# Optimization experiments

Hardware: AMD Instinct MI355X
Metric: run time of the kernel (lower is better)

Reference implementation:

```python
import jax, jax.numpy as jnp
import numpy as np

# Model dims (match init_kwargs)
N = 150            # n_constituents
P = 16             # len(params)
HID = 50           # hidden
DE = 14            # De
DO = 10            # Do
NT = 5             # n_targets
B = 256            # batch
NR = N * (N - 1)   # 22350 directed edges


def _linear_params(key, fan_in, fan_out):
    # torch.nn.Linear default init: U(-1/sqrt(fan_in), 1/sqrt(fan_in))
    k1, k2 = jax.random.split(key)
    lim = 1.0 / np.sqrt(fan_in)
    W = jax.random.uniform(k1, (fan_out, fan_in), minval=-lim, maxval=lim, dtype=jnp.float32)
    b = jax.random.uniform(k2, (fan_out,), minval=-lim, maxval=lim, dtype=jnp.float32)
    return W, b


def setup_inputs() -> dict:
    key = jax.random.key(0)
    ks = jax.random.split(key, 10)
    # Edge list: itertools.product(range(N), range(N)) with r != s; Rr one-hot on r, Rs on s.
    pairs = np.array([(r, s) for r in range(N) for s in range(N) if r != s], dtype=np.int32)
    recv = jnp.asarray(pairs[:, 0])  # [NR]
    send = jnp.asarray(pairs[:, 1])  # [NR]

    x = jax.random.normal(ks[0], (B, P, N), dtype=jnp.float32)

    fr1_w, fr1_b = _linear_params(ks[1], 2 * P, HID)
    fr2_w, fr2_b = _linear_params(ks[2], HID, HID // 2)
    fr3_w, fr3_b = _linear_params(ks[3], HID // 2, DE)
    fo1_w, fo1_b = _linear_params(ks[4], P + DE, HID)
    fo2_w, fo2_b = _linear_params(ks[5], HID, HID // 2)
    fo3_w, fo3_b = _linear_params(ks[6], HID // 2, DO)
    fc1_w, fc1_b = _linear_params(ks[7], DO * N, HID)
    fc2_w, fc2_b = _linear_params(ks[8], HID, HID // 2)
    fc3_w, fc3_b = _linear_params(ks[9], HID // 2, NT)

    return dict(x=x, recv=recv, send=send,
                fr1_w=fr1_w, fr1_b=fr1_b, fr2_w=fr2_w, fr2_b=fr2_b, fr3_w=fr3_w, fr3_b=fr3_b,
                fo1_w=fo1_w, fo1_b=fo1_b, fo2_w=fo2_w, fo2_b=fo2_b, fo3_w=fo3_w, fo3_b=fo3_b,
                fc1_w=fc1_w, fc1_b=fc1_b, fc2_w=fc2_w, fc2_b=fc2_b, fc3_w=fc3_w, fc3_b=fc3_b)


def reference(x, recv, send,
              fr1_w, fr1_b, fr2_w, fr2_b, fr3_w, fr3_b,
              fo1_w, fo1_b, fo2_w, fo2_b, fo3_w, fo3_b,
              fc1_w, fc1_b, fc2_w, fc2_b, fc3_w, fc3_b):
    relu = jax.nn.relu
    b = x.shape[0]
    # tmul(x, Rr/Rs) with one-hot Rr/Rs == gather along the node axis
    Orr = x[:, :, recv]                                   # (B, P, NR)
    Ors = x[:, :, send]                                   # (B, P, NR)
    Bm = jnp.concatenate([Orr, Ors], axis=1)              # (B, 2P, NR)
    Bm = jnp.transpose(Bm, (0, 2, 1))                     # (B, NR, 2P)
    # relational MLP fr (ReLU branch)
    h = relu(jnp.einsum('bef,hf->beh', Bm, fr1_w) + fr1_b)
    h = relu(jnp.einsum('beh,gh->beg', h, fr2_w) + fr2_b)
    E = relu(jnp.einsum('beg,dg->bed', h, fr3_w) + fr3_b)  # (B, NR, De)
    # tmul(E, Rr^T) == scatter-add edge effects onto receiver nodes
    Ebar = jnp.zeros((b, N, E.shape[-1]), x.dtype).at[:, recv].add(E)  # (B, N, De)
    C = jnp.concatenate([jnp.transpose(x, (0, 2, 1)), Ebar], axis=-1)  # (B, N, P+De)
    # object MLP fo
    h = relu(jnp.einsum('bnf,hf->bnh', C, fo1_w) + fo1_b)
    h = relu(jnp.einsum('bnh,gh->bng', h, fo2_w) + fo2_b)
    O = relu(jnp.einsum('bng,dg->bnd', h, fo3_w) + fo3_b)  # (B, N, Do)
    # classifier fc (sum_O=False: flatten N*Do)
    flat = O.reshape(b, N * O.shape[-1])
    h = relu(flat @ fc1_w.T + fc1_b)
    h = relu(h @ fc2_w.T + fc2_b)
    out = h @ fc3_w.T + fc3_b                              # (B, n_targets)
    return out
```

## Files before the change

kernel.cpp:

```cpp
#include <hip/hip_runtime.h>

#define N_   150
#define P_   16
#define DE_  14
#define DO_  10
#define NT_  5
#define B_   256
#define NRE  22350
#define H2_  25
#define HID_ 50
#define RPW  5

typedef float    f32x4 __attribute__((ext_vector_type(4)));
typedef _Float16 f16x8 __attribute__((ext_vector_type(8)));
typedef _Float16 f16x4 __attribute__((ext_vector_type(4)));

typedef f16x8 f16x8_a __attribute__((may_alias));
typedef f16x4 f16x4_a __attribute__((may_alias));
typedef int2  int2_a  __attribute__((may_alias));
typedef f32x4 f32x4_a __attribute__((may_alias));

#define EBAR_OFF 0u
#define O_OFF    2457600u
#define XT_OFF   3225600u
#define W1E_OFF  4454400u
#define W1O_OFF  4458496u
#define W2E_OFF  4462592u
#define W2O_OFF  4466688u
#define W3E_OFF  4470784u
#define W3O_OFF  4471808u
#define B1E_OFF  4472832u
#define B1O_OFF  4473088u
#define B2E_OFF  4473344u
#define B2O_OFF  4473472u
#define B3E_OFF  4473600u
#define B3O_OFF  4473664u

__global__ __launch_bounds__(256) void prep_kernel(
    const float* __restrict__ x,
    const float* __restrict__ fr1_w, const float* __restrict__ fr1_b,
    const float* __restrict__ fr2_w, const float* __restrict__ fr2_b,
    const float* __restrict__ fr3_w, const float* __restrict__ fr3_b,
    const float* __restrict__ fo1_w, const float* __restrict__ fo1_b,
    const float* __restrict__ fo2_w, const float* __restrict__ fo2_b,
    const float* __restrict__ fo3_w, const float* __restrict__ fo3_b,
    char* __restrict__ ws)
{
    int tid = blockIdx.x * 256 + threadIdx.x;
    if (tid < 614400) {
        int b = tid / 2400; int rr = tid - b * 2400;
        int n = rr >> 4, p = rr & 15;
        ((_Float16*)(ws + XT_OFF))[tid] = (_Float16)x[b * 2400 + p * N_ + n];
        return;
    }
    int t = tid - 614400;
    if (t < 2048) { int n = t >> 5, k = t & 31;
        ((_Float16*)(ws + W1E_OFF))[t] = (_Float16)((n < 50) ? fr1_w[n * 32 + k] : 0.f); return; }
    t -= 2048;
    if (t < 2048) { int n = t >> 5, k = t & 31;
        ((_Float16*)(ws + W1O_OFF))[t] = (_Float16)((n < 50 && k < 30) ? fo1_w[n * 30 + k] : 0.f); return; }
    t -= 2048;
    if (t < 2048) { int n = t >> 6, k = t & 63;
        ((_Float16*)(ws + W2E_OFF))[t] = (_Float16)((n < 25 && k < 50) ? fr2_w[n * 50 + k] : 0.f); return; }
    t -= 2048;
    if (t < 2048) { int n = t >> 6, k = t & 63;
        ((_Float16*)(ws + W2O_OFF))[t] = (_Float16)((n < 25 && k < 50) ? fo2_w[n * 50 + k] : 0.f); return; }
    t -= 2048;
    if (t < 512) { int n = t >> 5, k = t & 31;
        ((_Float16*)(ws + W3E_OFF))[t] = (_Float16)((n < 14 && k < 25) ? fr3_w[n * 25 + k] : 0.f); return; }
    t -= 512;
    if (t < 512) { int n = t >> 5, k = t & 31;
        ((_Float16*)(ws + W3O_OFF))[t] = (_Float16)((n < 10 && k < 25) ? fo3_w[n * 25 + k] : 0.f); return; }
    t -= 512;
    if (t < 64) { ((float*)(ws + B1E_OFF))[t] = (t < 50) ? fr1_b[t] : 0.f; return; }
    t -= 64;
    if (t < 64) { ((float*)(ws + B1O_OFF))[t] = (t < 50) ? fo1_b[t] : 0.f; return; }
    t -= 64;
    if (t < 32) { ((float*)(ws + B2E_OFF))[t] = (t < 25) ? fr2_b[t] : 0.f; return; }
    t -= 32;
    if (t < 32) { ((float*)(ws + B2O_OFF))[t] = (t < 25) ? fo2_b[t] : 0.f; return; }
    t -= 32;
    if (t < 16) { ((float*)(ws + B3E_OFF))[t] = (t < 14) ? fr3_b[t] : 0.f; return; }
    t -= 16;
    if (t < 16) { ((float*)(ws + B3O_OFF))[t] = (t < 10) ? fo3_b[t] : 0.f; return; }
}

__device__ __forceinline__ unsigned pk2(float a, float b) {
    auto p = __builtin_amdgcn_cvt_pkrtz(a, b);
    return __builtin_bit_cast(unsigned, p);
}
__device__ __forceinline__ unsigned pkmax0(unsigned x, unsigned z) {
    unsigned r;
    asm("v_pk_max_f16 %0, %1, %2" : "=v"(r) : "v"(x), "v"(z));
    return r;
}

template<int CTRL>
__device__ __forceinline__ float dppadd(float v) {
    int s = __builtin_amdgcn_update_dpp(0, __builtin_bit_cast(int, v), CTRL, 0xF, 0xF, true);
    return v + __builtin_bit_cast(float, s);
}
__device__ __forceinline__ float dpp_sum16(float v) {
    v = dppadd<0x121>(v);
    v = dppadd<0x122>(v);
    v = dppadd<0x124>(v);
    v = dppadd<0x128>(v);
    return v;
}

__global__ __launch_bounds__(256) void edge_kernel(char* __restrict__ ws)
{
    const _Float16* __restrict__ xT = (const _Float16*)(ws + XT_OFF);
    const _Float16* __restrict__ W1 = (const _Float16*)(ws + W1E_OFF);
    const _Float16* __restrict__ W2 = (const _Float16*)(ws + W2E_OFF);
    const _Float16* __restrict__ W3 = (const _Float16*)(ws + W3E_OFF);
    const float* __restrict__ b1 = (const float*)(ws + B1E_OFF);
    const float* __restrict__ b2 = (const float*)(ws + B2E_OFF);
    const float* __restrict__ b3 = (const float*)(ws + B3E_OFF);
    float* __restrict__ Ebar = (float*)(ws + EBAR_OFF);

    const int t = threadIdx.x, lane = t & 63, wid = t >> 6;
    const int e16 = lane & 15, g = lane >> 4;

    __shared__ __align__(16) char s_lds[4][6144];
    char* L = s_lds[wid];

    const int gw = blockIdx.x * 4 + wid;
    const int b  = gw / 30;
    const int r0 = (gw - b * 30) * RPW;

    f16x4 A1r[4], A1s[4];
#pragma unroll
    for (int nt = 0; nt < 4; ++nt) {
        A1r[nt] = *(const f16x4*)&W1[(nt * 16 + e16) * 32 + g * 4];
        A1s[nt] = *(const f16x4*)&W1[(nt * 16 + e16) * 32 + 16 + g * 4];
    }
    f16x8 A2f[2][2], A3f;
#pragma unroll
    for (int nt = 0; nt < 2; ++nt)
#pragma unroll
        for (int kt = 0; kt < 2; ++kt)
            A2f[nt][kt] = *(const f16x8*)&W2[(nt * 16 + e16) * 64 + kt * 32 + g * 8];
    A3f = *(const f16x8*)&W3[e16 * 32 + g * 8];

    f32x4 Cb1[4], Cb2[2], Cb3;
#pragma unroll
    for (int nt = 0; nt < 4; ++nt) Cb1[nt] = *(const f32x4*)&b1[nt * 16 + g * 4];
#pragma unroll
    for (int nt = 0; nt < 2; ++nt) Cb2[nt] = *(const f32x4*)&b2[nt * 16 + g * 4];
    Cb3 = *(const f32x4*)&b3[g * 4];

    const char* xTb = (const char*)xT + b * 4800;
    const int laneoff = e16 * 32 + g * 8;
    const int wsub = (g >> 1) * 256 + e16 * 16 + 8 * (g & 1);
    const int rsub = g * 256 + e16 * 16;
    const unsigned zu = 0;

    for (int rr = 0; rr < RPW; ++rr) {
        const int r = r0 + rr;

        f16x4 Bxr = *(const f16x4_a*)(xTb + r * 32 + g * 8);
        f32x4 H1P[4];
#pragma unroll
        for (int nt = 0; nt < 4; ++nt)
            H1P[nt] = __builtin_amdgcn_mfma_f32_16x16x16f16(A1r[nt], Bxr, Cb1[nt], 0, 0, 0);

        const int ktile = r >> 4, klane = r & 15;
        float ac0 = 0.f, ac1 = 0.f, ac2 = 0.f, ac3 = 0.f;

#pragma unroll 2
        for (int tile = 0; tile < 10; ++tile) {
            char* h1b = L + (tile & 1) * 3072;
            char* h2b = h1b + 2048;

            f16x4 Bxs = *(const f16x4_a*)(xTb + tile * 512 + laneoff);

#pragma unroll
            for (int nt = 0; nt < 4; ++nt) {
                f32x4 d1 = __builtin_amdgcn_mfma_f32_16x16x16f16(A1s[nt], Bxs, H1P[nt], 0, 0, 0);
                int2 pw;
                pw.x = (int)pkmax0(pk2(d1[0], d1[1]), zu);
                pw.y = (int)pkmax0(pk2(d1[2], d1[3]), zu);
                *(int2_a*)(h1b + nt * 512 + wsub) = pw;
            }

            f16x8 B2a = *(const f16x8_a*)(h1b + rsub);
            f16x8 B2b = *(const f16x8_a*)(h1b + 1024 + rsub);
#pragma unroll
            for (int nt = 0; nt < 2; ++nt) {
                f32x4 d2 = __builtin_amdgcn_mfma_f32_16x16x32_f16(A2f[nt][0], B2a, Cb2[nt], 0, 0, 0);
                d2 = __builtin_amdgcn_mfma_f32_16x16x32_f16(A2f[nt][1], B2b, d2, 0, 0, 0);
                int2 pw;
                pw.x = (int)pkmax0(pk2(d2[0], d2[1]), zu);
                pw.y = (int)pkmax0(pk2(d2[2], d2[3]), zu);
                *(int2_a*)(h2b + nt * 512 + wsub) = pw;
            }

            f16x8 B3f = *(const f16x8_a*)(h2b + rsub);
            f32x4 d3 = __builtin_amdgcn_mfma_f32_16x16x32_f16(A3f, B3f, Cb3, 0, 0, 0);

            float v0 = fmaxf(d3[0], 0.f), v1 = fmaxf(d3[1], 0.f);
            float v2 = fmaxf(d3[2], 0.f), v3 = fmaxf(d3[3], 0.f);
            if (tile == ktile || tile == 9) {
                bool kill = (tile == ktile && e16 == klane) || (tile == 9 && e16 >= 6);
                if (kill) { v0 = 0.f; v1 = 0.f; v2 = 0.f; v3 = 0.f; }
            }
            ac0 += v0; ac1 += v1; ac2 += v2; ac3 += v3;
        }

        ac0 = dpp_sum16(ac0); ac1 = dpp_sum16(ac1);
        ac2 = dpp_sum16(ac2); ac3 = dpp_sum16(ac3);
        if (e16 == 0) {
            f32x4 o = { ac0, ac1, ac2, ac3 };
            *(f32x4_a*)&Ebar[(b * 150 + r) * 16 + g * 4] = o;
        }
    }
}

__global__ __launch_bounds__(256) void obj_kernel(char* __restrict__ ws)
{
    const _Float16* __restrict__ xT = (const _Float16*)(ws + XT_OFF);
    const _Float16* __restrict__ W1 = (const _Float16*)(ws + W1O_OFF);
    const _Float16* __restrict__ W2 = (const _Float16*)(ws + W2O_OFF);
    const _Float16* __restrict__ W3 = (const _Float16*)(ws + W3O_OFF);
    const float* __restrict__ b1 = (const float*)(ws + B1O_OFF);
    const float* __restrict__ b2 = (const float*)(ws + B2O_OFF);
    const float* __restrict__ b3 = (const float*)(ws + B3O_OFF);
    const float* __restrict__ Ebar = (const float*)(ws + EBAR_OFF);
    _Float16* __restrict__ O = (_Float16*)(ws + O_OFF);

    const int t = threadIdx.x, lane = t & 63, wid = t >> 6;
    const int e16 = lane & 15, g = lane >> 4;

    __shared__ __align__(16) char s_lds[4][3072];
    char* ldsw = s_lds[wid];
    const int wsub = (g >> 1) * 256 + e16 * 16 + (g & 1) * 8;
    char*       h1w = ldsw + wsub;
    char*       h2w = ldsw + 2048 + wsub;
    const int rsub = g * 256 + e16 * 16;
    const char* h1r = ldsw + rsub;
    const char* h2r = ldsw + 2048 + rsub;

    f16x8 A1[4], A2[2][2], A3;
#pragma unroll
    for (int nt = 0; nt < 4; ++nt)
        A1[nt] = *(const f16x8*)&W1[(nt * 16 + e16) * 32 + g * 8];
#pragma unroll
    for (int nt = 0; nt < 2; ++nt)
#pragma unroll
        for (int kt = 0; kt < 2; ++kt)
            A2[nt][kt] = *(const f16x8*)&W2[(nt * 16 + e16) * 64 + kt * 32 + g * 8];
    A3 = *(const f16x8*)&W3[e16 * 32 + g * 8];

    f32x4 C1[4], C2[2];
#pragma unroll
    for (int nt = 0; nt < 4; ++nt) C1[nt] = *(const f32x4*)&b1[nt * 16 + g * 4];
#pragma unroll
    for (int nt = 0; nt < 2; ++nt) C2[nt] = *(const f32x4*)&b2[nt * 16 + g * 4];
    const float b3v = b3[e16];
    const f32x4 C3 = { b3v, b3v, b3v, b3v };
    const unsigned zu = 0;

    const int tile = blockIdx.x * 4 + wid;
    const int m = tile * 16 + e16;

    f16x8 Bf;
    if (g < 2) {
        Bf = *(const f16x8*)&xT[m * 16 + g * 8];
    } else {
        const float* ep = &Ebar[m * 16 + (g & 1) * 8];
        f32x4 u0 = *(const f32x4_a*)ep;
        f32x4 u1 = *(const f32x4_a*)(ep + 4);
        uint4 uw;
        uw.x = pk2(u0[0], u0[1]); uw.y = pk2(u0[2], u0[3]);
        uw.z = pk2(u1[0], u1[1]); uw.w = pk2(u1[2], u1[3]);
        Bf = __builtin_bit_cast(f16x8, uw);
    }

#pragma unroll
    for (int nt = 0; nt < 4; ++nt) {
        f32x4 a = __builtin_amdgcn_mfma_f32_16x16x32_f16(A1[nt], Bf, C1[nt], 0, 0, 0);
        int2 pw;
        pw.x = (int)pkmax0(pk2(a[0], a[1]), zu);
        pw.y = (int)pkmax0(pk2(a[2], a[3]), zu);
        *(int2_a*)(h1w + nt * 512) = pw;
    }
    f16x8 B2a = *(const f16x8_a*)(h1r);
    f16x8 B2b = *(const f16x8_a*)(h1r + 1024);
#pragma unroll
    for (int nt = 0; nt < 2; ++nt) {
        f32x4 a = __builtin_amdgcn_mfma_f32_16x16x32_f16(A2[nt][0], B2a, C2[nt], 0, 0, 0);
        a = __builtin_amdgcn_mfma_f32_16x16x32_f16(A2[nt][1], B2b, a, 0, 0, 0);
        int2 pw;
        pw.x = (int)pkmax0(pk2(a[0], a[1]), zu);
        pw.y = (int)pkmax0(pk2(a[2], a[3]), zu);
        *(int2_a*)(h2w + nt * 512) = pw;
    }
    f16x8 Af3 = *(const f16x8_a*)(h2r);
    f32x4 acc3 = __builtin_amdgcn_mfma_f32_16x16x32_f16(Af3, A3, C3, 0, 0, 0);

    if (e16 < DO_) {
#pragma unroll
        for (int v = 0; v < 4; ++v)
            O[(tile * 16 + g * 4 + v) * DO_ + e16] = (_Float16)fmaxf(acc3[v], 0.f);
    }
}

__global__ __launch_bounds__(256) void classifier_kernel(
    const _Float16* __restrict__ O,
    const float* __restrict__ fc1_w, const float* __restrict__ fc1_b,
    const float* __restrict__ fc2_w, const float* __restrict__ fc2_b,
    const float* __restrict__ fc3_w, const float* __restrict__ fc3_b,
    float* __restrict__ out)
{
    __shared__ float s_o[N_ * DO_];
    __shared__ float s_part[4][HID_];
    __shared__ float s_h1[HID_];
    __shared__ float s_h2[H2_];

    const int b = blockIdx.x;
    const int t = threadIdx.x;
    const int lane = t & 63, w = t >> 6;

    const _Float16* Ob = O + b * (N_ * DO_);
    for (int k = t; k < N_ * DO_; k += 256) s_o[k] = (float)Ob[k];
    __syncthreads();

    float acc[HID_];
#pragma unroll
    for (int i = 0; i < HID_; ++i) acc[i] = 0.0f;

    for (int kb = 0; kb < N_ * DO_; kb += 256) {
        int k = kb + t;
        if (k < N_ * DO_) {
            float o = s_o[k];
#pragma unroll
            for (int i = 0; i < HID_; ++i)
                acc[i] = fmaf(fc1_w[i * (N_ * DO_) + k], o, acc[i]);
        }
    }

#pragma unroll
    for (int i = 0; i < HID_; ++i) {
        float v = acc[i];
#pragma unroll
        for (int off = 32; off >= 1; off >>= 1) v += __shfl_xor(v, off);
        if (lane == i) s_part[w][i] = v;
    }
    __syncthreads();

    if (t < HID_) {
        float v = s_part[0][t] + s_part[1][t] + s_part[2][t] + s_part[3][t] + fc1_b[t];
        s_h1[t] = fmaxf(v, 0.0f);
    }
    __syncthreads();
    if (t < H2_) {
        float a = fc2_b[t];
#pragma unroll
        for (int k = 0; k < HID_; ++k) a = fmaf(fc2_w[t * HID_ + k], s_h1[k], a);
        s_h2[t] = fmaxf(a, 0.0f);
    }
    __syncthreads();
    if (t < NT_) {
        float a = fc3_b[t];
#pragma unroll
        for (int k = 0; k < H2_; ++k) a = fmaf(fc3_w[t * H2_ + k], s_h2[k], a);
        out[b * NT_ + t] = a;
    }
}

extern "C" void kernel_launch(void* const* d_in, const int* in_sizes, int n_in,
                              void* d_out, int out_size, void* d_ws, size_t ws_size,
                              hipStream_t stream) {
    const float* x     = (const float*)d_in[0];
    const float* fr1_w = (const float*)d_in[3];
    const float* fr1_b = (const float*)d_in[4];
    const float* fr2_w = (const float*)d_in[5];
    const float* fr2_b = (const float*)d_in[6];
    const float* fr3_w = (const float*)d_in[7];
    const float* fr3_b = (const float*)d_in[8];
    const float* fo1_w = (const float*)d_in[9];
    const float* fo1_b = (const float*)d_in[10];
    const float* fo2_w = (const float*)d_in[11];
    const float* fo2_b = (const float*)d_in[12];
    const float* fo3_w = (const float*)d_in[13];
    const float* fo3_b = (const float*)d_in[14];
    const float* fc1_w = (const float*)d_in[15];
    const float* fc1_b = (const float*)d_in[16];
    const float* fc2_w = (const float*)d_in[17];
    const float* fc2_b = (const float*)d_in[18];
    const float* fc3_w = (const float*)d_in[19];
    const float* fc3_b = (const float*)d_in[20];

    char* ws = (char*)d_ws;
    float* out = (float*)d_out;

    prep_kernel<<<2437, 256, 0, stream>>>(x, fr1_w, fr1_b, fr2_w, fr2_b, fr3_w, fr3_b,
                                          fo1_w, fo1_b, fo2_w, fo2_b, fo3_w, fo3_b, ws);
    edge_kernel<<<1920, 256, 0, stream>>>(ws);
    obj_kernel<<<600, 256, 0, stream>>>(ws);
    classifier_kernel<<<B_, 256, 0, stream>>>((const _Float16*)(ws + O_OFF),
                                              fc1_w, fc1_b, fc2_w, fc2_b, fc3_w, fc3_b, out);
}
```

Before: 111.8 us.

## Replace LDS round-trip between edge MLP layers with in-register lane transposes

In the edge kernel, the MFMA output of layers 1 and 2 is no longer written to shared memory and read back in the B-operand layout. The reordering is now done in registers with permlane32_swap plus xor-16 shuffles, which removes the LDS buffers and the store/load latency on the critical path. The receivers handled per wave also drop from 5 to 2, and the grid grows from 1920 to 4800 blocks to give more parallelism. In exchange each tile does extra cross-lane operations, and each wave re-does its per-wave weight and bias loads more often.

```diff
diff --git a/kernel.cpp b/kernel.cpp
--- a/kernel.cpp
+++ b/kernel.cpp
@@ -9,7 +9,7 @@
 #define NRE  22350
 #define H2_  25
 #define HID_ 50
-#define RPW  5
+#define RPW  2
 
 typedef float    f32x4 __attribute__((ext_vector_type(4)));
 typedef _Float16 f16x8 __attribute__((ext_vector_type(8)));
@@ -89,10 +89,10 @@
     auto p = __builtin_amdgcn_cvt_pkrtz(a, b);
     return __builtin_bit_cast(unsigned, p);
 }
-__device__ __forceinline__ unsigned pkmax0(unsigned x, unsigned z) {
+__device__ __forceinline__ int pkmax0(unsigned x, unsigned z) {
     unsigned r;
     asm("v_pk_max_f16 %0, %1, %2" : "=v"(r) : "v"(x), "v"(z));
-    return r;
+    return (int)r;
 }
 
 template<int CTRL>
@@ -106,6 +106,15 @@
     v = dppadd<0x124>(v);
     v = dppadd<0x128>(v);
     return v;
+}
+
+__device__ __forceinline__ void xpose4(int A, int B, bool hi16, int& Y0, int& Y1) {
+    auto s = __builtin_amdgcn_permlane32_swap(A, B, false, false);
+    int va = s[0], vb = s[1];
+    int sa = __shfl_xor(va, 16);
+    int sb = __shfl_xor(vb, 16);
+    Y0 = hi16 ? sb : va;
+    Y1 = hi16 ? vb : sa;
 }
 
 __global__ __launch_bounds__(256) void edge_kernel(char* __restrict__ ws)
@@ -121,13 +130,11 @@
 
     const int t = threadIdx.x, lane = t & 63, wid = t >> 6;
     const int e16 = lane & 15, g = lane >> 4;
-
-    __shared__ __align__(16) char s_lds[4][6144];
-    char* L = s_lds[wid];
+    const bool hi16 = (lane & 16) != 0;
 
     const int gw = blockIdx.x * 4 + wid;
-    const int b  = gw / 30;
-    const int r0 = (gw - b * 30) * RPW;
+    const int b  = gw / 75;
+    const int r0 = (gw - b * 75) * RPW;
 
     f16x4 A1r[4], A1s[4];
 #pragma unroll
@@ -152,8 +159,6 @@
 
     const char* xTb = (const char*)xT + b * 4800;
     const int laneoff = e16 * 32 + g * 8;
-    const int wsub = (g >> 1) * 256 + e16 * 16 + 8 * (g & 1);
-    const int rsub = g * 256 + e16 * 16;
     const unsigned zu = 0;
 
     for (int rr = 0; rr < RPW; ++rr) {
@@ -170,33 +175,50 @@
 
 #pragma unroll 2
         for (int tile = 0; tile < 10; ++tile) {
-            char* h1b = L + (tile & 1) * 3072;
-            char* h2b = h1b + 2048;
-
             f16x4 Bxs = *(const f16x4_a*)(xTb + tile * 512 + laneoff);
 
+            int P[4][2];
 #pragma unroll
             for (int nt = 0; nt < 4; ++nt) {
                 f32x4 d1 = __builtin_amdgcn_mfma_f32_16x16x16f16(A1s[nt], Bxs, H1P[nt], 0, 0, 0);
-                int2 pw;
-                pw.x = (int)pkmax0(pk2(d1[0], d1[1]), zu);
-                pw.y = (int)pkmax0(pk2(d1[2], d1[3]), zu);
-                *(int2_a*)(h1b + nt * 512 + wsub) = pw;
+                P[nt][0] = pkmax0(pk2(d1[0], d1[1]), zu);
+                P[nt][1] = pkmax0(pk2(d1[2], d1[3]), zu);
             }
 
-            f16x8 B2a = *(const f16x8_a*)(h1b + rsub);
-            f16x8 B2b = *(const f16x8_a*)(h1b + 1024 + rsub);
+            uint4 B2w0, B2w1;
+            {
+                int y00, y10, y01, y11;
+                xpose4(P[0][0], P[1][0], hi16, y00, y10);
+                xpose4(P[0][1], P[1][1], hi16, y01, y11);
+                B2w0.x = (unsigned)y00; B2w0.y = (unsigned)y01;
+                B2w0.z = (unsigned)y10; B2w0.w = (unsigned)y11;
+                xpose4(P[2][0], P[3][0], hi16, y00, y10);
+                xpose4(P[2][1], P[3][1], hi16, y01, y11);
+                B2w1.x = (unsigned)y00; B2w1.y = (unsigned)y01;
+                B2w1.z = (unsigned)y10; B2w1.w = (unsigned)y11;
+            }
+            f16x8 B2a = __builtin_bit_cast(f16x8, B2w0);
+            f16x8 B2b = __builtin_bit_cast(f16x8, B2w1);
+
+            int P2[2][2];
 #pragma unroll
             for (int nt = 0; nt < 2; ++nt) {
                 f32x4 d2 = __builtin_amdgcn_mfma_f32_16x16x32_f16(A2f[nt][0], B2a, Cb2[nt], 0, 0, 0);
                 d2 = __builtin_amdgcn_mfma_f32_16x16x32_f16(A2f[nt][1], B2b, d2, 0, 0, 0);
-                int2 pw;
-                pw.x = (int)pkmax0(pk2(d2[0], d2[1]), zu);
-                pw.y = (int)pkmax0(pk2(d2[2], d2[3]), zu);
-                *(int2_a*)(h2b + nt * 512 + wsub) = pw;
+                P2[nt][0] = pkmax0(pk2(d2[0], d2[1]), zu);
+                P2[nt][1] = pkmax0(pk2(d2[2], d2[3]), zu);
             }
 
-            f16x8 B3f = *(const f16x8_a*)(h2b + rsub);
+            uint4 B3w;
+            {
+                int z00, z10, z01, z11;
+                xpose4(P2[0][0], P2[1][0], hi16, z00, z10);
+                xpose4(P2[0][1], P2[1][1], hi16, z01, z11);
+                B3w.x = (unsigned)z00; B3w.y = (unsigned)z01;
+                B3w.z = (unsigned)z10; B3w.w = (unsigned)z11;
+            }
+            f16x8 B3f = __builtin_bit_cast(f16x8, B3w);
+
             f32x4 d3 = __builtin_amdgcn_mfma_f32_16x16x32_f16(A3f, B3f, Cb3, 0, 0, 0);
 
             float v0 = fmaxf(d3[0], 0.f), v1 = fmaxf(d3[1], 0.f);
@@ -281,8 +303,8 @@
     for (int nt = 0; nt < 4; ++nt) {
         f32x4 a = __builtin_amdgcn_mfma_f32_16x16x32_f16(A1[nt], Bf, C1[nt], 0, 0, 0);
         int2 pw;
-        pw.x = (int)pkmax0(pk2(a[0], a[1]), zu);
-        pw.y = (int)pkmax0(pk2(a[2], a[3]), zu);
+        pw.x = pkmax0(pk2(a[0], a[1]), zu);
+        pw.y = pkmax0(pk2(a[2], a[3]), zu);
         *(int2_a*)(h1w + nt * 512) = pw;
     }
     f16x8 B2a = *(const f16x8_a*)(h1r);
@@ -292,8 +314,8 @@
         f32x4 a = __builtin_amdgcn_mfma_f32_16x16x32_f16(A2[nt][0], B2a, C2[nt], 0, 0, 0);
         a = __builtin_amdgcn_mfma_f32_16x16x32_f16(A2[nt][1], B2b, a, 0, 0, 0);
         int2 pw;
-        pw.x = (int)pkmax0(pk2(a[0], a[1]), zu);
-        pw.y = (int)pkmax0(pk2(a[2], a[3]), zu);
+        pw.x = pkmax0(pk2(a[0], a[1]), zu);
+        pw.y = pkmax0(pk2(a[2], a[3]), zu);
         *(int2_a*)(h2w + nt * 512) = pw;
     }
     f16x8 Af3 = *(const f16x8_a*)(h2r);
@@ -397,7 +419,7 @@
 
     prep_kernel<<<2437, 256, 0, stream>>>(x, fr1_w, fr1_b, fr2_w, fr2_b, fr3_w, fr3_b,
                                           fo1_w, fo1_b, fo2_w, fo2_b, fo3_w, fo3_b, ws);
-    edge_kernel<<<1920, 256, 0, stream>>>(ws);
+    edge_kernel<<<4800, 256, 0, stream>>>(ws);
     obj_kernel<<<600, 256, 0, stream>>>(ws);
     classifier_kernel<<<B_, 256, 0, stream>>>((const _Float16*)(ws + O_OFF),
                                               fc1_w, fc1_b, fc2_w, fc2_b, fc3_w, fc3_b, out);
```

Measured after the change: 129.3 us. +15.7%, slower.
